# Performance work log

Measured on AMD Instinct MI355X. Metric: run time of the kernel, lower is better.

The kernel has to match this reference:

```python
import jax, jax.numpy as jnp
import numpy as np

L, H, V, T, E = 12, 12, 50257, 1024, 768
DH = E // H
EPS = 1e-5


def _ln(x, g, b):
    mu = jnp.mean(x, axis=-1, keepdims=True)
    var = jnp.mean(jnp.square(x - mu), axis=-1, keepdims=True)
    return g * (x - mu) * jax.lax.rsqrt(var + EPS) + b


def _gelu(x):
    # tanh-approx gelu as in the source
    return 0.5 * x * (1.0 + jnp.tanh(jnp.sqrt(2.0 / jnp.pi) * (x + 0.044715 * jnp.power(x, 3))))


def setup_inputs() -> dict:
    key = jax.random.key(0)
    ks = jax.random.split(key, 12)
    s = 0.02
    return {
        "x": jax.random.randint(ks[0], (8, T), 0, V),
        "tok_emb": jax.random.normal(ks[1], (V, E), jnp.float32) * s,
        "pos_emb": jax.random.normal(ks[2], (T, E), jnp.float32) * s,
        "ln1_g": jnp.ones((L, E), jnp.float32),
        "ln1_b": jnp.zeros((L, E), jnp.float32),
        "Wqkv": jax.random.normal(ks[3], (L, E, 3 * E), jnp.float32) * s,
        "bqkv": jnp.zeros((L, 3 * E), jnp.float32),
        "Wo": jax.random.normal(ks[4], (L, E, E), jnp.float32) * s,
        "bo": jnp.zeros((L, E), jnp.float32),
        "ln2_g": jnp.ones((L, E), jnp.float32),
        "ln2_b": jnp.zeros((L, E), jnp.float32),
        "W1": jax.random.normal(ks[5], (L, E, 4 * E), jnp.float32) * s,
        "b1": jnp.zeros((L, 4 * E), jnp.float32),
        "W2": jax.random.normal(ks[6], (L, 4 * E, E), jnp.float32) * s,
        "b2": jnp.zeros((L, E), jnp.float32),
        "lnf_g": jnp.ones((E,), jnp.float32),
        "lnf_b": jnp.zeros((E,), jnp.float32),
    }


def _gpt2(x, tok_emb, pos_emb, ln1_g, ln1_b, Wqkv, bqkv, Wo, bo,
          ln2_g, ln2_b, W1, b1, W2, b2, lnf_g, lnf_b):
    B, S = x.shape
    h = tok_emb[x] + pos_emb[:S][None, :, :]  # [B,S,E]
    mask = (jnp.arange(S)[:, None] >= jnp.arange(S)[None, :]).astype(jnp.float32)  # [S,S]
    mask = mask[None, None]  # [1,1,S,S]
    scale = jax.lax.rsqrt(jnp.float32(DH))
    for l in range(L):
        a = _ln(h, ln1_g[l], ln1_b[l])
        qkv = jnp.einsum('bse,ef->bsf', a, Wqkv[l]) + bqkv[l]
        q, k, v = jnp.split(qkv, 3, axis=-1)
        q = q.reshape(B, S, H, DH).transpose(0, 2, 1, 3)
        k = k.reshape(B, S, H, DH).transpose(0, 2, 1, 3)
        v = v.reshape(B, S, H, DH).transpose(0, 2, 1, 3)
        w = jnp.einsum('bhqd,bhkd->bhqk', q, k) * scale
        w = w * mask - 1e10 * (1.0 - mask)
        w = jax.nn.softmax(w, axis=-1)
        ctx = jnp.einsum('bhqk,bhkd->bhqd', w, v)
        ctx = ctx.transpose(0, 2, 1, 3).reshape(B, S, E)
        h = h + jnp.einsum('bse,ef->bsf', ctx, Wo[l]) + bo[l]
        a2 = _ln(h, ln2_g[l], ln2_b[l])
        ff = _gelu(jnp.einsum('bse,ef->bsf', a2, W1[l]) + b1[l])
        h = h + jnp.einsum('bsf,fe->bse', ff, W2[l]) + b2[l]
    h = _ln(h, lnf_g, lnf_b)
    last = h[:, -1, :]  # [B,E]
    return jnp.matmul(last, tok_emb.T)  # [B,V]


def reference(x, tok_emb, pos_emb, ln1_g, ln1_b, Wqkv, bqkv, Wo, bo,
              ln2_g, ln2_b, W1, b1, W2, b2, lnf_g, lnf_b):
    return _gpt2(x, tok_emb, pos_emb, ln1_g, ln1_b, Wqkv, bqkv, Wo, bo,
                 ln2_g, ln2_b, W1, b1, W2, b2, lnf_g, lnf_b)
```

## Files before the change

### kernel.cpp

```cpp
#include <hip/hip_runtime.h>
#include <math.h>

#define LNUM 12
#define HNUM 12
#define EMB 768
#define TSEQ 1024
#define BBATCH 8
#define VOCAB 50257
#define NTOK (BBATCH*TSEQ)

typedef unsigned short u16;
typedef __bf16 bf16_8 __attribute__((ext_vector_type(8)));
typedef float f32x4 __attribute__((ext_vector_type(4)));

__device__ __forceinline__ u16 f2bf(float f){
  unsigned u = __float_as_uint(f);
  u += 0x7fffu + ((u >> 16) & 1u);
  return (u16)(u >> 16);
}
__device__ __forceinline__ float wred(float v){
  #pragma unroll
  for (int m = 32; m; m >>= 1) v += __shfl_xor(v, m, 64);
  return v;
}

#define GLOAD_LDS16(g, l) \
  __builtin_amdgcn_global_load_lds((const __attribute__((address_space(1))) void*)(g), \
                                   (__attribute__((address_space(3))) void*)(l), 16, 0, 0)

template<int N> struct WCst { static constexpr int val = N; };

__global__ __launch_bounds__(256) void tcvt_kernel(const float* __restrict__ src,
                                                   u16* __restrict__ dst, int K, int N){
  __shared__ float tile[32][33];
  size_t off = (size_t)blockIdx.z * K * N;
  const float* s = src + off;
  u16* d = dst + off;
  int n0 = blockIdx.x * 32, k0 = blockIdx.y * 32;
  int tx = threadIdx.x & 31, ty = threadIdx.x >> 5;
  #pragma unroll
  for (int i = 0; i < 4; i++)
    tile[ty + i*8][tx] = s[(size_t)(k0 + ty + i*8) * N + n0 + tx];
  __syncthreads();
  #pragma unroll
  for (int i = 0; i < 4; i++){
    int n = ty + i*8;
    d[(size_t)(n0 + n) * K + k0 + tx] = f2bf(tile[tx][n]);
  }
}

__global__ __launch_bounds__(256) void embed_kernel(const int* __restrict__ x,
    const float* __restrict__ tok, const float* __restrict__ pos, float* __restrict__ h){
  int row = blockIdx.x;
  int t = row & (TSEQ - 1);
  int id = x[row];
  const float* te = tok + (size_t)id * EMB;
  const float* pe = pos + (size_t)t * EMB;
  float* hr = h + (size_t)row * EMB;
  for (int i = threadIdx.x; i < EMB; i += 256) hr[i] = te[i] + pe[i];
}

template<int OBF, int LAST>
__global__ __launch_bounds__(256) void ln_kernel(const float* __restrict__ x,
    const float* __restrict__ g, const float* __restrict__ b, void* __restrict__ out){
  int orow, row;
  if (LAST){ orow = blockIdx.x; row = blockIdx.x * TSEQ + (TSEQ - 1); }
  else     { orow = row = blockIdx.x; }
  const float* xr = x + (size_t)row * EMB;
  int tid = threadIdx.x;
  int wave = tid >> 6, lane = tid & 63;
  float v[3];
  float s = 0.f;
  #pragma unroll
  for (int i = 0; i < 3; i++){ v[i] = xr[tid + i*256]; s += v[i]; }
  __shared__ float red[4];
  s = wred(s);
  if (lane == 0) red[wave] = s;
  __syncthreads();
  float mu = (red[0] + red[1] + red[2] + red[3]) * (1.f / EMB);
  float ss = 0.f;
  #pragma unroll
  for (int i = 0; i < 3; i++){ float d = v[i] - mu; ss += d * d; }
  __syncthreads();
  ss = wred(ss);
  if (lane == 0) red[wave] = ss;
  __syncthreads();
  float var = (red[0] + red[1] + red[2] + red[3]) * (1.f / EMB);
  float rs = rsqrtf(var + 1e-5f);
  #pragma unroll
  for (int i = 0; i < 3; i++){
    int e = tid + i*256;
    float o = g[e] * (v[i] - mu) * rs + b[e];
    if (OBF) ((u16*)out)[(size_t)orow * EMB + e] = f2bf(o);
    else     ((float*)out)[(size_t)orow * EMB + e] = o;
  }
}

template<int EPI>
__global__ __launch_bounds__(256, 2) void gemm_ring(const u16* __restrict__ A,
    const u16* __restrict__ Bt, const float* __restrict__ bias,
    const float* __restrict__ resid, void* __restrict__ outp, int K, int N){
  constexpr int SLOTE = 16 * 512;
  constexpr int LOADS = 4;
  __shared__ __align__(16) u16 lds[4 * SLOTE];
  const int tid  = threadIdx.x;
  const int wave = tid >> 6, lane = tid & 63;
  const int q15  = lane & 15, ko = lane >> 4;
  const int wm   = wave >> 1, wn = wave & 1;
  const int nwg = (int)gridDim.x, cpx = nwg >> 3, d = (int)blockIdx.x;
  const int orig = (d & 7) * cpx + (d >> 3);
  const int NBN = N >> 7;
  const int bn = orig % NBN, bm = orig / NBN;
  const int NT = K >> 5;

  const u16* gA = A  + (size_t)(bm*128 + wave*16 + q15) * K + ko * 8;
  const u16* gB = Bt + (size_t)(bn*128 + wave*16 + q15) * K + ko * 8;

#define STAGE(tt, so) do { \
    int _t = (tt); \
    GLOAD_LDS16(gA + (size_t)_t*32,                 lds + (so) + wave*512); \
    GLOAD_LDS16(gA + (size_t)_t*32 + (size_t)64*K,  lds + (so) + (wave+4)*512); \
    GLOAD_LDS16(gB + (size_t)_t*32,                 lds + (so) + (8+wave)*512); \
    GLOAD_LDS16(gB + (size_t)_t*32 + (size_t)64*K,  lds + (so) + (12+wave)*512); \
  } while (0)

  f32x4 acc[4][4];
  #pragma unroll
  for (int i = 0; i < 4; i++)
    #pragma unroll
    for (int j = 0; j < 4; j++){ f32x4 z = {0.f,0.f,0.f,0.f}; acc[i][j] = z; }

  auto tile = [&](int t, auto wc, bool dostage, bool dosync){
    if (dostage) STAGE(t + 3, ((t + 3) & 3) * SLOTE);
    const u16* sl = lds + (t & 3) * SLOTE;
    bf16_8 af[4], bfr[4];
    #pragma unroll
    for (int mi = 0; mi < 4; mi++)
      af[mi] = *(const bf16_8*)(sl + (wm*4 + mi) * 512 + lane * 8);
    #pragma unroll
    for (int ni = 0; ni < 4; ni++)
      bfr[ni] = *(const bf16_8*)(sl + (8 + wn*4 + ni) * 512 + lane * 8);
    __builtin_amdgcn_s_setprio(1);
    #pragma unroll
    for (int mi = 0; mi < 4; mi++)
      #pragma unroll
      for (int ni = 0; ni < 4; ni++)
        acc[mi][ni] = __builtin_amdgcn_mfma_f32_16x16x32_bf16(af[mi], bfr[ni], acc[mi][ni], 0, 0, 0);
    __builtin_amdgcn_s_setprio(0);
    if (dosync){
      asm volatile("s_waitcnt vmcnt(%0)" :: "n"(decltype(wc)::val) : "memory");
      __builtin_amdgcn_sched_barrier(0);
      __builtin_amdgcn_s_barrier();
      __builtin_amdgcn_sched_barrier(0);
    }
  };

  STAGE(0, 0);
  STAGE(1, SLOTE);
  STAGE(2, 2*SLOTE);
  asm volatile("s_waitcnt vmcnt(%0)" :: "n"(2 * LOADS) : "memory");
  __builtin_amdgcn_sched_barrier(0);
  __builtin_amdgcn_s_barrier();
  __builtin_amdgcn_sched_barrier(0);

  for (int t = 0; t < NT - 3; ++t) tile(t, WCst<2 * LOADS>{}, true, true);
  tile(NT - 3, WCst<LOADS>{}, false, true);
  tile(NT - 2, WCst<0>{},     false, true);
  tile(NT - 1, WCst<0>{},     false, false);
#undef STAGE

  const int colb = bn*128 + wn*64;
  const int rowb = bm*128 + wm*64;
  #pragma unroll
  for (int ni = 0; ni < 4; ni++){
    int col = colb + ni*16 + q15;
    float bv = bias[col];
    #pragma unroll
    for (int mi = 0; mi < 4; mi++){
      #pragma unroll
      for (int j = 0; j < 4; j++){
        int row = rowb + mi*16 + ko*4 + j;
        float v = acc[mi][ni][j] + bv;
        if (EPI == 1) v += resid[(size_t)row * N + col];
        if (EPI == 2){
          float y = 0.7978845608028654f * (v + 0.044715f * v * v * v);
          float e = __expf(fminf(2.f * y, 80.f));
          v = v * e / (e + 1.f);
        }
        if (EPI == 3 && col < 768) v *= 0.125f;
        if (EPI == 2 || EPI == 3) ((u16*)outp)[(size_t)row * N + col] = f2bf(v);
        else                      ((float*)outp)[(size_t)row * N + col] = v;
      }
    }
  }
}

__global__ __launch_bounds__(256) void vtrans_kernel(const u16* __restrict__ qkvb,
                                                     u16* __restrict__ vt){
  int wave = threadIdx.x >> 6, lane = threadIdx.x & 63;
  int bh = blockIdx.y, b = bh / HNUM, h = bh - b * HNUM;
  int t0 = blockIdx.x * 16 + wave * 4;
  const u16* src = qkvb + (size_t)b * TSEQ * 2304 + 1536 + h * 64 + lane;
  unsigned long long w = 0;
  #pragma unroll
  for (int i = 0; i < 4; i++)
    w |= (unsigned long long)src[(size_t)(t0 + i) * 2304] << (16 * i);
  *(unsigned long long*)(vt + ((size_t)bh * 64 + lane) * TSEQ + t0) = w;
}

__global__ __launch_bounds__(256, 2) void attn_mfma(const u16* __restrict__ qkvb,
                                                    const u16* __restrict__ vt,
                                                    u16* __restrict__ ctx){
  __shared__ u16 plds[4][64][40];
  const int wave = threadIdx.x >> 6, lane = threadIdx.x & 63;
  const int g = lane >> 4, q15 = lane & 15;
  const int bh = blockIdx.y, b = bh / HNUM, h = bh - b * HNUM;
  const int q0 = ((int)gridDim.x - 1 - (int)blockIdx.x) * 256 + wave * 64;
  const u16* qk  = qkvb + (size_t)b * TSEQ * 2304 + h * 64;
  const u16* vtb = vt + (size_t)bh * 64 * TSEQ;

#define LOADKV(kb_, kd, vd) do { \
    _Pragma("unroll") \
    for (int _kf = 0; _kf < 2; _kf++) \
      _Pragma("unroll") \
      for (int _kc = 0; _kc < 2; _kc++) \
        kd[_kf][_kc] = *(const bf16_8*)(qk + (size_t)((kb_) + _kf*16 + q15) * 2304 + 768 + _kc*32 + g*8); \
    _Pragma("unroll") \
    for (int _dc = 0; _dc < 4; _dc++) \
      vd[_dc] = *(const bf16_8*)(vtb + (size_t)(_dc*16 + q15) * TSEQ + (kb_) + g*8); \
  } while (0)

  bf16_8 qfr[4][2];
  #pragma unroll
  for (int qf = 0; qf < 4; qf++)
    #pragma unroll
    for (int kc = 0; kc < 2; kc++)
      qfr[qf][kc] = *(const bf16_8*)(qk + (size_t)(q0 + qf*16 + q15) * 2304 + kc*32 + g*8);

  f32x4 oacc[4][4];
  #pragma unroll
  for (int i = 0; i < 4; i++)
    #pragma unroll
    for (int j = 0; j < 4; j++){ f32x4 z = {0.f,0.f,0.f,0.f}; oacc[i][j] = z; }
  float mx[4] = {-1e30f,-1e30f,-1e30f,-1e30f}, lsum[4] = {0.f,0.f,0.f,0.f};

  const int kbmax = q0 + 32;
  bf16_8 kcur[2][2], vcur[4];
  LOADKV(0, kcur, vcur);

  for (int kb = 0; kb <= kbmax; kb += 32){
    bf16_8 knxt[2][2], vnxt[4];
    if (kb < kbmax) LOADKV(kb + 32, knxt, vnxt);

    f32x4 s[2][4];
    #pragma unroll
    for (int kf = 0; kf < 2; kf++)
      #pragma unroll
      for (int qf = 0; qf < 4; qf++){
        f32x4 z = {0.f,0.f,0.f,0.f};
        z = __builtin_amdgcn_mfma_f32_16x16x32_bf16(kcur[kf][0], qfr[qf][0], z, 0, 0, 0);
        z = __builtin_amdgcn_mfma_f32_16x16x32_bf16(kcur[kf][1], qfr[qf][1], z, 0, 0, 0);
        s[kf][qf] = z;
      }

    if (kb + 31 > q0){
      #pragma unroll
      for (int kf = 0; kf < 2; kf++)
        #pragma unroll
        for (int qf = 0; qf < 4; qf++)
          #pragma unroll
          for (int j = 0; j < 4; j++)
            if (kb + kf*16 + g*4 + j > q0 + qf*16 + q15) s[kf][qf][j] = -1e30f;
    }

    #pragma unroll
    for (int qf = 0; qf < 4; qf++){
      float sm = -1e30f;
      #pragma unroll
      for (int kf = 0; kf < 2; kf++)
        #pragma unroll
        for (int j = 0; j < 4; j++) sm = fmaxf(sm, s[kf][qf][j]);
      sm = fmaxf(sm, __shfl_xor(sm, 16, 64));
      sm = fmaxf(sm, __shfl_xor(sm, 32, 64));
      float mn = fmaxf(mx[qf], sm);
      float c = __expf(mx[qf] - mn);
      mx[qf] = mn;
      float ps = 0.f;
      unsigned long long pw[2];
      #pragma unroll
      for (int kf = 0; kf < 2; kf++){
        unsigned long long w = 0;
        #pragma unroll
        for (int j = 0; j < 4; j++){
          float p = __expf(s[kf][qf][j] - mn);
          ps += p;
          w |= (unsigned long long)f2bf(p) << (16 * j);
        }
        pw[kf] = w;
      }
      ps += __shfl_xor(ps, 16, 64);
      ps += __shfl_xor(ps, 32, 64);
      lsum[qf] = lsum[qf] * c + ps;
      *(unsigned long long*)&plds[wave][qf*16 + q15][g*4]      = pw[0];
      *(unsigned long long*)&plds[wave][qf*16 + q15][16 + g*4] = pw[1];
      #pragma unroll
      for (int j = 0; j < 4; j++){
        float cr = __shfl(c, g*4 + j, 64);
        #pragma unroll
        for (int dc = 0; dc < 4; dc++) oacc[qf][dc][j] *= cr;
      }
    }

    asm volatile("s_waitcnt lgkmcnt(0)" ::: "memory");
    __builtin_amdgcn_sched_barrier(0);

    bf16_8 pa[4];
    #pragma unroll
    for (int qf = 0; qf < 4; qf++)
      pa[qf] = *(const bf16_8*)&plds[wave][qf*16 + q15][g*8];
    #pragma unroll
    for (int qf = 0; qf < 4; qf++)
      #pragma unroll
      for (int dc = 0; dc < 4; dc++)
        oacc[qf][dc] = __builtin_amdgcn_mfma_f32_16x16x32_bf16(pa[qf], vcur[dc], oacc[qf][dc], 0, 0, 0);

    if (kb < kbmax){
      #pragma unroll
      for (int kf = 0; kf < 2; kf++)
        #pragma unroll
        for (int kc = 0; kc < 2; kc++) kcur[kf][kc] = knxt[kf][kc];
      #pragma unroll
      for (int dc = 0; dc < 4; dc++) vcur[dc] = vnxt[dc];
    }
  }
#undef LOADKV

  u16* cb = ctx + ((size_t)(b * TSEQ + q0)) * EMB + h * 64;
  #pragma unroll
  for (int qf = 0; qf < 4; qf++){
    float inv = 1.f / lsum[qf];
    #pragma unroll
    for (int j = 0; j < 4; j++){
      float ir = __shfl(inv, g*4 + j, 64);
      int row = qf*16 + g*4 + j;
      #pragma unroll
      for (int dc = 0; dc < 4; dc++)
        cb[(size_t)row * EMB + dc*16 + q15] = f2bf(oacc[qf][dc][j] * ir);
    }
  }
}

__global__ __launch_bounds__(256) void logits_kernel(const float* __restrict__ last,
    const float* __restrict__ tok, float* __restrict__ out){
  __shared__ float ls[BBATCH * EMB];
  for (int i = threadIdx.x; i < BBATCH * EMB; i += 256) ls[i] = last[i];
  __syncthreads();
  int wave = threadIdx.x >> 6, lane = threadIdx.x & 63;
  int v = blockIdx.x * 4 + wave;
  if (v >= VOCAB) return;
  const float* tp = tok + (size_t)v * EMB;
  float acc[BBATCH];
  #pragma unroll
  for (int b = 0; b < BBATCH; b++) acc[b] = 0.f;
  #pragma unroll
  for (int i = 0; i < EMB/64; i++){
    float tv = tp[i*64 + lane];
    #pragma unroll
    for (int b = 0; b < BBATCH; b++) acc[b] += tv * ls[b*EMB + i*64 + lane];
  }
  #pragma unroll
  for (int b = 0; b < BBATCH; b++){
    float r = wred(acc[b]);
    if (lane == 0) out[(size_t)b * VOCAB + v] = r;
  }
}

extern "C" void kernel_launch(void* const* d_in, const int* in_sizes, int n_in,
                              void* d_out, int out_size, void* d_ws, size_t ws_size,
                              hipStream_t stream){
  const int*   x    = (const int*)  d_in[0];
  const float* tok  = (const float*)d_in[1];
  const float* pos  = (const float*)d_in[2];
  const float* ln1g = (const float*)d_in[3];
  const float* ln1b = (const float*)d_in[4];
  const float* Wqkv = (const float*)d_in[5];
  const float* bqkv = (const float*)d_in[6];
  const float* Wo   = (const float*)d_in[7];
  const float* bo   = (const float*)d_in[8];
  const float* ln2g = (const float*)d_in[9];
  const float* ln2b = (const float*)d_in[10];
  const float* W1   = (const float*)d_in[11];
  const float* b1   = (const float*)d_in[12];
  const float* W2   = (const float*)d_in[13];
  const float* b2   = (const float*)d_in[14];
  const float* lnfg = (const float*)d_in[15];
  const float* lnfb = (const float*)d_in[16];

  char* p = (char*)d_ws;
  u16* wqkvT = (u16*)p;  p += (size_t)LNUM*2304*768*2;
  u16* woT   = (u16*)p;  p += (size_t)LNUM*768*768*2;
  u16* w1T   = (u16*)p;  p += (size_t)LNUM*3072*768*2;
  u16* w2T   = (u16*)p;  p += (size_t)LNUM*768*3072*2;
  float* h   = (float*)p; p += (size_t)NTOK*EMB*4;
  u16* abuf  = (u16*)p;  p += (size_t)NTOK*EMB*2;
  void* tmp  = (void*)p; p += (size_t)NTOK*2304*4;
  u16* vt    = (u16*)p;  p += (size_t)BBATCH*HNUM*64*TSEQ*2;
  float* lastb = (float*)p; p += (size_t)BBATCH*EMB*4;
  if (ws_size < (size_t)(p - (char*)d_ws)) return;

  tcvt_kernel<<<dim3(2304/32, 768/32, LNUM), 256, 0, stream>>>(Wqkv, wqkvT, 768, 2304);
  tcvt_kernel<<<dim3(768/32,  768/32, LNUM), 256, 0, stream>>>(Wo,   woT,   768, 768);
  tcvt_kernel<<<dim3(3072/32, 768/32, LNUM), 256, 0, stream>>>(W1,   w1T,   768, 3072);
  tcvt_kernel<<<dim3(768/32, 3072/32, LNUM), 256, 0, stream>>>(W2,   w2T,   3072, 768);
  embed_kernel<<<NTOK, 256, 0, stream>>>(x, tok, pos, h);

  u16* qkvb = (u16*)tmp;
  u16* ff   = (u16*)tmp;
  for (int l = 0; l < LNUM; l++){
    ln_kernel<1,0><<<NTOK, 256, 0, stream>>>(h, ln1g + l*EMB, ln1b + l*EMB, abuf);
    gemm_ring<3><<<(2304/128)*(NTOK/128), 256, 0, stream>>>(
        abuf, wqkvT + (size_t)l*2304*768, bqkv + (size_t)l*2304, nullptr, qkvb, 768, 2304);
    vtrans_kernel<<<dim3(TSEQ/16, BBATCH*HNUM), 256, 0, stream>>>(qkvb, vt);
    attn_mfma<<<dim3(TSEQ/256, BBATCH*HNUM), 256, 0, stream>>>(qkvb, vt, abuf);
    gemm_ring<1><<<(768/128)*(NTOK/128), 256, 0, stream>>>(
        abuf, woT + (size_t)l*768*768, bo + (size_t)l*768, h, h, 768, 768);
    ln_kernel<1,0><<<NTOK, 256, 0, stream>>>(h, ln2g + l*EMB, ln2b + l*EMB, abuf);
    gemm_ring<2><<<(3072/128)*(NTOK/128), 256, 0, stream>>>(
        abuf, w1T + (size_t)l*3072*768, b1 + (size_t)l*3072, nullptr, ff, 768, 3072);
    gemm_ring<1><<<(768/128)*(NTOK/128), 256, 0, stream>>>(
        ff, w2T + (size_t)l*768*3072, b2 + (size_t)l*768, h, h, 3072, 768);
  }
  ln_kernel<0,1><<<BBATCH, 256, 0, stream>>>(h, lnfg, lnfb, lastb);
  logits_kernel<<<(VOCAB + 3)/4, 256, 0, stream>>>(lastb, tok, (float*)d_out);
}
```

Before: 4.552 ms.

## Replace 4-stage 128x128 GEMM ring with 8-wave 128x256 double-buffered ping-pong GEMM

The GEMM kernel moves from 256 threads computing a 128x128 tile with a four-slot LDS ring over K=32 steps to 512 threads (8 waves) computing a 128x256 tile. K advances 64 per step in two 32-wide phases, and the LDS is double-buffered. Each phase reads its fragments, issues the next stage's global-to-LDS loads, then runs the MFMAs between barriers. The wider tile reuses each A load across more columns and gives more waves per block to hide latency, but it roughly halves the number of blocks for the N=768 GEMMs and adds more barriers per K step.

```diff
diff --git a/kernel.cpp b/kernel.cpp
--- a/kernel.cpp
+++ b/kernel.cpp
@@ -27,8 +27,6 @@
 #define GLOAD_LDS16(g, l) \
   __builtin_amdgcn_global_load_lds((const __attribute__((address_space(1))) void*)(g), \
                                    (__attribute__((address_space(3))) void*)(l), 16, 0, 0)
-
-template<int N> struct WCst { static constexpr int val = N; };
 
 __global__ __launch_bounds__(256) void tcvt_kernel(const float* __restrict__ src,
                                                    u16* __restrict__ dst, int K, int N){
@@ -97,79 +95,83 @@
 }
 
 template<int EPI>
-__global__ __launch_bounds__(256, 2) void gemm_ring(const u16* __restrict__ A,
+__global__ __launch_bounds__(512, 2) void gemm8p(const u16* __restrict__ A,
     const u16* __restrict__ Bt, const float* __restrict__ bias,
     const float* __restrict__ resid, void* __restrict__ outp, int K, int N){
-  constexpr int SLOTE = 16 * 512;
-  constexpr int LOADS = 4;
-  __shared__ __align__(16) u16 lds[4 * SLOTE];
+  constexpr int BUFE = 48 * 512;
+  __shared__ __align__(16) u16 lds[2 * BUFE];
   const int tid  = threadIdx.x;
   const int wave = tid >> 6, lane = tid & 63;
   const int q15  = lane & 15, ko = lane >> 4;
-  const int wm   = wave >> 1, wn = wave & 1;
-  const int nwg = (int)gridDim.x, cpx = nwg >> 3, d = (int)blockIdx.x;
-  const int orig = (d & 7) * cpx + (d >> 3);
-  const int NBN = N >> 7;
+  const int wm   = wave >> 2, wn = wave & 3;
+  const int nwg = (int)gridDim.x, cpx = nwg >> 3, dd = (int)blockIdx.x;
+  const int orig = (dd & 7) * cpx + (dd >> 3);
+  const int NBN = N >> 8;
   const int bn = orig % NBN, bm = orig / NBN;
-  const int NT = K >> 5;
+  const int NT = K >> 6;
 
   const u16* gA = A  + (size_t)(bm*128 + wave*16 + q15) * K + ko * 8;
-  const u16* gB = Bt + (size_t)(bn*128 + wave*16 + q15) * K + ko * 8;
-
-#define STAGE(tt, so) do { \
-    int _t = (tt); \
-    GLOAD_LDS16(gA + (size_t)_t*32,                 lds + (so) + wave*512); \
-    GLOAD_LDS16(gA + (size_t)_t*32 + (size_t)64*K,  lds + (so) + (wave+4)*512); \
-    GLOAD_LDS16(gB + (size_t)_t*32,                 lds + (so) + (8+wave)*512); \
-    GLOAD_LDS16(gB + (size_t)_t*32 + (size_t)64*K,  lds + (so) + (12+wave)*512); \
+  const u16* gB = Bt + (size_t)(bn*256 + wave*32 + q15) * K + ko * 8;
+
+#define SBATCH(tt, kc) do { \
+    int _t = (tt), _kc = (kc); \
+    u16* _b = lds + (_t & 1) * BUFE; \
+    int _k = _t * 64 + _kc * 32; \
+    GLOAD_LDS16(gA + _k,                 _b + (wave*2 + _kc) * 512); \
+    GLOAD_LDS16(gB + _k,                 _b + (16 + wave*4 + _kc) * 512); \
+    GLOAD_LDS16(gB + _k + (size_t)16*K,  _b + (16 + wave*4 + 2 + _kc) * 512); \
   } while (0)
 
+#define ENDSYNC(n) do { \
+    asm volatile("s_waitcnt vmcnt(" #n ")" ::: "memory"); \
+    __builtin_amdgcn_sched_barrier(0); \
+    __builtin_amdgcn_s_barrier(); \
+    __builtin_amdgcn_sched_barrier(0); \
+  } while (0)
+
   f32x4 acc[4][4];
   #pragma unroll
   for (int i = 0; i < 4; i++)
     #pragma unroll
     for (int j = 0; j < 4; j++){ f32x4 z = {0.f,0.f,0.f,0.f}; acc[i][j] = z; }
 
-  auto tile = [&](int t, auto wc, bool dostage, bool dosync){
-    if (dostage) STAGE(t + 3, ((t + 3) & 3) * SLOTE);
-    const u16* sl = lds + (t & 3) * SLOTE;
-    bf16_8 af[4], bfr[4];
+  auto phase = [&](int t, int ks, bool dostage){
+    const u16* bb = lds + (t & 1) * BUFE;
+    bf16_8 af[4], bf[4];
     #pragma unroll
     for (int mi = 0; mi < 4; mi++)
-      af[mi] = *(const bf16_8*)(sl + (wm*4 + mi) * 512 + lane * 8);
+      af[mi] = *(const bf16_8*)(bb + ((wm*4 + mi)*2 + ks) * 512 + lane * 8);
     #pragma unroll
     for (int ni = 0; ni < 4; ni++)
-      bfr[ni] = *(const bf16_8*)(sl + (8 + wn*4 + ni) * 512 + lane * 8);
+      bf[ni] = *(const bf16_8*)(bb + (16 + (wn*4 + ni)*2 + ks) * 512 + lane * 8);
+    if (dostage) SBATCH(t + 1, ks);
+    __builtin_amdgcn_sched_barrier(0);
+    __builtin_amdgcn_s_barrier();
+    asm volatile("s_waitcnt lgkmcnt(0)" ::: "memory");
+    __builtin_amdgcn_sched_barrier(0);
     __builtin_amdgcn_s_setprio(1);
     #pragma unroll
     for (int mi = 0; mi < 4; mi++)
       #pragma unroll
       for (int ni = 0; ni < 4; ni++)
-        acc[mi][ni] = __builtin_amdgcn_mfma_f32_16x16x32_bf16(af[mi], bfr[ni], acc[mi][ni], 0, 0, 0);
+        acc[mi][ni] = __builtin_amdgcn_mfma_f32_16x16x32_bf16(af[mi], bf[ni], acc[mi][ni], 0, 0, 0);
     __builtin_amdgcn_s_setprio(0);
-    if (dosync){
-      asm volatile("s_waitcnt vmcnt(%0)" :: "n"(decltype(wc)::val) : "memory");
-      __builtin_amdgcn_sched_barrier(0);
-      __builtin_amdgcn_s_barrier();
-      __builtin_amdgcn_sched_barrier(0);
-    }
   };
 
-  STAGE(0, 0);
-  STAGE(1, SLOTE);
-  STAGE(2, 2*SLOTE);
-  asm volatile("s_waitcnt vmcnt(%0)" :: "n"(2 * LOADS) : "memory");
-  __builtin_amdgcn_sched_barrier(0);
-  __builtin_amdgcn_s_barrier();
-  __builtin_amdgcn_sched_barrier(0);
-
-  for (int t = 0; t < NT - 3; ++t) tile(t, WCst<2 * LOADS>{}, true, true);
-  tile(NT - 3, WCst<LOADS>{}, false, true);
-  tile(NT - 2, WCst<0>{},     false, true);
-  tile(NT - 1, WCst<0>{},     false, false);
-#undef STAGE
-
-  const int colb = bn*128 + wn*64;
+  SBATCH(0, 0);
+  SBATCH(0, 1);
+  ENDSYNC(3);
+
+  for (int t = 0; t < NT - 1; ++t){
+    phase(t, 0, true);  ENDSYNC(3);
+    phase(t, 1, true);  ENDSYNC(3);
+  }
+  phase(NT - 1, 0, false); ENDSYNC(0);
+  phase(NT - 1, 1, false);
+#undef SBATCH
+#undef ENDSYNC
+
+  const int colb = bn*256 + wn*64;
   const int rowb = bm*128 + wm*64;
   #pragma unroll
   for (int ni = 0; ni < 4; ni++){
@@ -418,16 +420,16 @@
   u16* ff   = (u16*)tmp;
   for (int l = 0; l < LNUM; l++){
     ln_kernel<1,0><<<NTOK, 256, 0, stream>>>(h, ln1g + l*EMB, ln1b + l*EMB, abuf);
-    gemm_ring<3><<<(2304/128)*(NTOK/128), 256, 0, stream>>>(
+    gemm8p<3><<<(NTOK/128)*(2304/256), 512, 0, stream>>>(
         abuf, wqkvT + (size_t)l*2304*768, bqkv + (size_t)l*2304, nullptr, qkvb, 768, 2304);
     vtrans_kernel<<<dim3(TSEQ/16, BBATCH*HNUM), 256, 0, stream>>>(qkvb, vt);
     attn_mfma<<<dim3(TSEQ/256, BBATCH*HNUM), 256, 0, stream>>>(qkvb, vt, abuf);
-    gemm_ring<1><<<(768/128)*(NTOK/128), 256, 0, stream>>>(
+    gemm8p<1><<<(NTOK/128)*(768/256), 512, 0, stream>>>(
         abuf, woT + (size_t)l*768*768, bo + (size_t)l*768, h, h, 768, 768);
     ln_kernel<1,0><<<NTOK, 256, 0, stream>>>(h, ln2g + l*EMB, ln2b + l*EMB, abuf);
-    gemm_ring<2><<<(3072/128)*(NTOK/128), 256, 0, stream>>>(
+    gemm8p<2><<<(NTOK/128)*(3072/256), 512, 0, stream>>>(
         abuf, w1T + (size_t)l*3072*768, b1 + (size_t)l*3072, nullptr, ff, 768, 3072);
-    gemm_ring<1><<<(768/128)*(NTOK/128), 256, 0, stream>>>(
+    gemm8p<1><<<(NTOK/128)*(768/256), 512, 0, stream>>>(
         ff, w2T + (size_t)l*768*3072, b2 + (size_t)l*768, h, h, 3072, 768);
   }
   ln_kernel<0,1><<<BBATCH, 256, 0, stream>>>(h, lnfg, lnfb, lastb);
```

After: 4.456 ms. 1.02x faster.
